# Performance work log

Measured on AMD Instinct MI355X. Metric: run time of the kernel, lower is better.

Reference implementation:

```python
import jax, jax.numpy as jnp
import numpy as np

N_NODES = 100000
N_EDGES = 800000
N_GRAPHS = 16
NFEAT = 128
NHID = 128
NCLASS = 2


def setup_inputs() -> dict:
    key = jax.random.key(0)
    k1, k2, k3, k4, k5, k6, k7 = jax.random.split(key, 7)
    x = jax.random.normal(k1, (N_NODES, NFEAT), dtype=jnp.float32)
    edge_index = jax.random.randint(k2, (2, N_EDGES), 0, N_NODES, dtype=jnp.int64)
    batch = jnp.sort(jax.random.randint(k3, (N_NODES,), 0, N_GRAPHS, dtype=jnp.int64))
    # GCNConv params (glorot-ish scale)
    W1 = jax.random.normal(k4, (NFEAT, NHID), dtype=jnp.float32) / np.sqrt(NFEAT)
    b1 = jnp.zeros((NHID,), dtype=jnp.float32)
    W2 = jax.random.normal(k5, (NHID, NCLASS), dtype=jnp.float32) / np.sqrt(NHID)
    b2 = jnp.zeros((NCLASS,), dtype=jnp.float32)
    return {"x": x, "edge_index": edge_index, "batch": batch,
            "W1": W1, "b1": b1, "W2": W2, "b2": b2}


def _prep_edges(edge_index, n):
    """Add self-loops and compute symmetric GCN normalization."""
    loop = jnp.arange(n, dtype=edge_index.dtype)
    row = jnp.concatenate([edge_index[0], loop])  # source
    col = jnp.concatenate([edge_index[1], loop])  # target
    deg = jax.ops.segment_sum(jnp.ones_like(col, dtype=jnp.float32), col, num_segments=n)
    dinv = jnp.where(deg > 0, jax.lax.rsqrt(deg), 0.0)
    norm = dinv[row] * dinv[col]  # [E+N]
    return row, col, norm


def _gcn_conv(x, row, col, norm, W, b):
    h = x @ W                                  # [N, out]
    msg = h[row] * norm[:, None]               # gather + scale, [E+N, out]
    out = jax.ops.segment_sum(msg, col, num_segments=x.shape[0])  # scatter-add
    return out + b


def reference(x, edge_index, batch, W1, b1, W2, b2):
    n = x.shape[0]
    row, col, norm = _prep_edges(edge_index, n)
    h = jax.nn.relu(_gcn_conv(x, row, col, norm, W1, b1))
    # dropout is identity at inference
    h = _gcn_conv(h, row, col, norm, W2, b2)
    # global_mean_pool over graph ids
    sums = jax.ops.segment_sum(h, batch, num_segments=N_GRAPHS)          # [G, nclass]
    cnts = jax.ops.segment_sum(jnp.ones((n,), h.dtype), batch, num_segments=N_GRAPHS)
    pooled = sums / jnp.maximum(cnts, 1.0)[:, None]
    return jax.nn.log_softmax(pooled, axis=1)
```

## Files before the change

kernel.cpp:

```cpp
#include <hip/hip_runtime.h>
#include <hip/hip_bf16.h>

#define N_NODES 100000
#define N_EDGES 800000
#define N_GRAPHS 16
#define NFEAT 128
#define NHID 128
#define NCLASS 2

#define SCAN_CHUNK 2048
#define NCHUNK ((N_NODES + SCAN_CHUNK - 1) / SCAN_CHUNK)

#define GEMM_BLOCKS 512
#define N_CHUNKS (N_NODES / 16)

#define FILL_BINS 8
#define FILL_SLICES 128
#define FILL_BIN_W (N_NODES / FILL_BINS)
#define FILL_SLICE_E (N_EDGES / FILL_SLICES)

#define P2_BLOCKS 512
#define P2_TPB 1024
#define P2_WAVES (P2_BLOCKS * (P2_TPB / 64))
#define P2_PER ((N_NODES + P2_WAVES - 1) / P2_WAVES)

typedef unsigned int uint32;
typedef __attribute__((ext_vector_type(8))) short short8;
typedef __attribute__((ext_vector_type(4))) float f32x4;
typedef __attribute__((ext_vector_type(2))) float f32x2;

__device__ __forceinline__ unsigned short f2bf(float f) {
  unsigned u = __float_as_uint(f);
  unsigned r = (u + 0x7fffu + ((u >> 16) & 1u)) >> 16;
  return (unsigned short)r;
}
__device__ __forceinline__ uint32 bfpack(float a, float b) {
  return (uint32)f2bf(a) | ((uint32)f2bf(b) << 16);
}
__device__ __forceinline__ float bflo(uint32 u) { return __uint_as_float(u << 16); }
__device__ __forceinline__ float bfhi(uint32 u) { return __uint_as_float(u & 0xffff0000u); }

__global__ void k_deg(const int* __restrict__ ei, int* __restrict__ deg) {
  int e = blockIdx.x * blockDim.x + threadIdx.x;
  if (e < N_EDGES) atomicAdd(&deg[ei[N_EDGES + e]], 1);
}

__global__ void k_scan1(const int* __restrict__ deg, int* __restrict__ csum,
                        float* __restrict__ dinv) {
  __shared__ int lds[256];
  int b = blockIdx.x, t = threadIdx.x;
  int base = b * SCAN_CHUNK + t * 8;
  int s = 0;
#pragma unroll
  for (int k = 0; k < 8; ++k) {
    int i = base + k;
    int d = (i < N_NODES) ? deg[i] : 0;
    if (i < N_NODES) dinv[i] = rsqrtf((float)d + 1.0f);
    s += d;
  }
  lds[t] = s;
  __syncthreads();
  for (int off = 128; off > 0; off >>= 1) {
    if (t < off) lds[t] += lds[t + off];
    __syncthreads();
  }
  if (t == 0) csum[b] = lds[0];
}

__global__ void k_scan3(const int* __restrict__ deg, const int* __restrict__ csum,
                        int* __restrict__ offsets, int* __restrict__ cursor) {
  __shared__ int lds[256];
  __shared__ int soff;
  int b = blockIdx.x, t = threadIdx.x;
  if (t == 0) {
    int run = 0;
    for (int i = 0; i < b; ++i) run += csum[i];
    soff = run;
  }
  int base = b * SCAN_CHUNK + t * 8;
  int v[8];
  int s = 0;
#pragma unroll
  for (int k = 0; k < 8; ++k) {
    int i = base + k;
    v[k] = (i < N_NODES) ? deg[i] : 0;
    s += v[k];
  }
  lds[t] = s;
  __syncthreads();
  int total = s;
  for (int off = 1; off < 256; off <<= 1) {
    int x = (t >= off) ? lds[t - off] : 0;
    __syncthreads();
    lds[t] += x;
    __syncthreads();
  }
  int run = lds[t] - total + soff;
#pragma unroll
  for (int k = 0; k < 8; ++k) {
    int i = base + k;
    if (i < N_NODES) { offsets[i] = run; cursor[i] = run; }
    run += v[k];
  }
}

__global__ __launch_bounds__(256) void k_fill(const int* __restrict__ ei,
                                              int* __restrict__ cursor,
                                              int* __restrict__ csr_row) {
  int bin = blockIdx.x & (FILL_BINS - 1);
  int slice = blockIdx.x >> 3;
  int lo = bin * FILL_BIN_W;
  int hi = lo + FILL_BIN_W;
  int e0 = slice * FILL_SLICE_E;
  int e1 = e0 + FILL_SLICE_E;
  for (int e = e0 + threadIdx.x; e < e1; e += 256) {
    int c = ei[N_EDGES + e];
    if (c >= lo && c < hi) {
      int r = ei[e];
      int p = atomicAdd(&cursor[c], 1);
      csr_row[p] = r;
    }
  }
}

__global__ __launch_bounds__(256, 2) void k_gemm_mfma(const float* __restrict__ x,
                                                      const float* __restrict__ W1,
                                                      const float* __restrict__ dinv,
                                                      unsigned char* __restrict__ xw8) {
  __shared__ __align__(16) unsigned short Wt[128 * 136];
  int t = threadIdx.x;
  for (int i = t; i < 4096; i += 256) {
    float4 w4 = ((const float4*)W1)[i];
    int k = i >> 5;
    int n0 = (i & 31) * 4;
    Wt[(n0 + 0) * 136 + k] = f2bf(w4.x);
    Wt[(n0 + 1) * 136 + k] = f2bf(w4.y);
    Wt[(n0 + 2) * 136 + k] = f2bf(w4.z);
    Wt[(n0 + 3) * 136 + k] = f2bf(w4.w);
  }
  __syncthreads();

  int lane = t & 63;
  int c = lane & 15;
  int quad = lane >> 4;
  short8 b[4][8];
#pragma unroll
  for (int kt = 0; kt < 4; ++kt)
#pragma unroll
    for (int nt = 0; nt < 8; ++nt)
      b[kt][nt] = *(const short8*)&Wt[(nt * 16 + c) * 136 + kt * 32 + quad * 8];

  int wave = blockIdx.x * 4 + (t >> 6);
  for (int chunk = wave; chunk < N_CHUNKS; chunk += GEMM_BLOCKS * 4) {
    const float* xr = x + (size_t)(chunk * 16 + c) * 128 + quad * 8;
    short8 a[4];
#pragma unroll
    for (int kt = 0; kt < 4; ++kt) {
      float4 f0 = *(const float4*)(xr + kt * 32);
      float4 f1 = *(const float4*)(xr + kt * 32 + 4);
      short8 v;
      v[0] = (short)f2bf(f0.x); v[1] = (short)f2bf(f0.y);
      v[2] = (short)f2bf(f0.z); v[3] = (short)f2bf(f0.w);
      v[4] = (short)f2bf(f1.x); v[5] = (short)f2bf(f1.y);
      v[6] = (short)f2bf(f1.z); v[7] = (short)f2bf(f1.w);
      a[kt] = v;
    }
    f32x4 acc[8];
#pragma unroll
    for (int nt = 0; nt < 8; ++nt) acc[nt] = (f32x4)(0.f);
#pragma unroll
    for (int kt = 0; kt < 4; ++kt)
#pragma unroll
      for (int nt = 0; nt < 8; ++nt)
        acc[nt] = __builtin_amdgcn_mfma_f32_16x16x32_bf16(a[kt], b[kt][nt], acc[nt], 0, 0, 0);

    int rbase = chunk * 16 + quad * 4;
    float d0 = dinv[rbase + 0], d1 = dinv[rbase + 1];
    float d2 = dinv[rbase + 2], d3 = dinv[rbase + 3];
#pragma unroll
    for (int nt = 0; nt < 8; ++nt) {
      int cb = nt * 16 + c;
      float v0 = acc[nt][0] * d0, v1 = acc[nt][1] * d1;
      float v2 = acc[nt][2] * d2, v3 = acc[nt][3] * d3;
      int p01 = __builtin_amdgcn_cvt_pk_fp8_f32(v0, v1, 0, false);
      int p23 = __builtin_amdgcn_cvt_pk_fp8_f32(v2, v3, 0, false);
      xw8[(size_t)(rbase + 0) * 128 + cb] = (unsigned char)(p01 & 0xff);
      xw8[(size_t)(rbase + 1) * 128 + cb] = (unsigned char)((p01 >> 8) & 0xff);
      xw8[(size_t)(rbase + 2) * 128 + cb] = (unsigned char)(p23 & 0xff);
      xw8[(size_t)(rbase + 3) * 128 + cb] = (unsigned char)((p23 >> 8) & 0xff);
    }
  }
}

__global__ __launch_bounds__(256) void k_conv1(const unsigned char* __restrict__ xw8,
                                               const int* __restrict__ csr_row,
                                               const int* __restrict__ offsets,
                                               const int* __restrict__ deg,
                                               const float* __restrict__ dinv,
                                               const float* __restrict__ b1,
                                               const float* __restrict__ W2,
                                               float2* __restrict__ h2) {
  int t = threadIdx.x;
  int lane = t & 63;
  int j = lane & 15;
  int gbase = lane & 48;
  int node = blockIdx.x * 16 + (t >> 4);

  int st = offsets[node];
  int cnt = deg[node];

  int ci = min(j, cnt);
  int rj = (ci == 0) ? node : csr_row[st + ci - 1];

  f32x2 acc2[4];
#pragma unroll
  for (int k = 0; k < 4; ++k) acc2[k] = (f32x2)(0.f);

  const uint2* rowp = (const uint2*)xw8;

#pragma unroll
  for (int i = 0; i < 16; ++i) {
    int r = __shfl(rj, gbase + i, 64);
    uint2 u = rowp[(size_t)r * 16 + j];
    if (i > cnt) { u.x = 0u; u.y = 0u; }
    acc2[0] += __builtin_amdgcn_cvt_pk_f32_fp8(u.x, false);
    acc2[1] += __builtin_amdgcn_cvt_pk_f32_fp8(u.x, true);
    acc2[2] += __builtin_amdgcn_cvt_pk_f32_fp8(u.y, false);
    acc2[3] += __builtin_amdgcn_cvt_pk_f32_fp8(u.y, true);
  }

  for (int s = 16; s <= cnt; s += 16) {
    int idx = s + j;
    int ci2 = min(idx, cnt);
    int rj2 = csr_row[st + ci2 - 1];
#pragma unroll
    for (int i = 0; i < 16; ++i) {
      int r = __shfl(rj2, gbase + i, 64);
      uint2 u = rowp[(size_t)r * 16 + j];
      if (s + i > cnt) { u.x = 0u; u.y = 0u; }
      acc2[0] += __builtin_amdgcn_cvt_pk_f32_fp8(u.x, false);
      acc2[1] += __builtin_amdgcn_cvt_pk_f32_fp8(u.x, true);
      acc2[2] += __builtin_amdgcn_cvt_pk_f32_fp8(u.y, false);
      acc2[3] += __builtin_amdgcn_cvt_pk_f32_fp8(u.y, true);
    }
  }

  float dc = dinv[node];
  float4 bA = *(const float4*)(b1 + j * 8);
  float4 bB = *(const float4*)(b1 + j * 8 + 4);
  float o[8];
  o[0] = fmaxf(acc2[0][0] * dc + bA.x, 0.f) * dc;
  o[1] = fmaxf(acc2[0][1] * dc + bA.y, 0.f) * dc;
  o[2] = fmaxf(acc2[1][0] * dc + bA.z, 0.f) * dc;
  o[3] = fmaxf(acc2[1][1] * dc + bA.w, 0.f) * dc;
  o[4] = fmaxf(acc2[2][0] * dc + bB.x, 0.f) * dc;
  o[5] = fmaxf(acc2[2][1] * dc + bB.y, 0.f) * dc;
  o[6] = fmaxf(acc2[3][0] * dc + bB.z, 0.f) * dc;
  o[7] = fmaxf(acc2[3][1] * dc + bB.w, 0.f) * dc;

  const float2* W2v = (const float2*)W2;
  float q0 = 0.f, q1 = 0.f;
#pragma unroll
  for (int k = 0; k < 8; ++k) {
    float2 wv = W2v[j * 8 + k];
    q0 += o[k] * wv.x;
    q1 += o[k] * wv.y;
  }
#pragma unroll
  for (int m = 1; m < 16; m <<= 1) {
    q0 += __shfl_xor(q0, m, 64);
    q1 += __shfl_xor(q1, m, 64);
  }
  if (j == 0) h2[node] = make_float2(q0, q1);
}

__global__ __launch_bounds__(P2_TPB) void k_conv2pool(const float2* __restrict__ h2,
                                                      const int* __restrict__ csr_row,
                                                      const int* __restrict__ offsets,
                                                      const int* __restrict__ deg,
                                                      const float* __restrict__ dinv,
                                                      const int* __restrict__ batch,
                                                      float* __restrict__ partials) {
  __shared__ float sacc[N_GRAPHS * 2];
  int t = threadIdx.x;
  if (t < N_GRAPHS * 2) sacc[t] = 0.f;
  __syncthreads();
  int lane = t & 63;
  int grp = lane >> 4;
  int j = lane & 15;
  int w = blockIdx.x * (P2_TPB / 64) + (t >> 6);
  int n0 = w * P2_PER;
  int n1 = min(n0 + P2_PER, N_NODES);
  float p0 = 0.f, p1 = 0.f;
  int gcur = -1;
  for (int nb = n0; nb < n1; nb += 4) {
    int node = nb + grp;
    bool valid = node < n1;
    int st = 0, cnt = -1;
    if (valid) { st = offsets[node]; cnt = deg[node]; }
    float a0 = 0.f, a1 = 0.f;
    for (int s = 0; s <= cnt; s += 16) {
      int idx = s + j;
      if (idx <= cnt) {
        int r = (idx == 0) ? node : csr_row[st + idx - 1];
        float2 v = h2[r];
        a0 += v.x;
        a1 += v.y;
      }
    }
#pragma unroll
    for (int m = 1; m < 16; m <<= 1) {
      a0 += __shfl_xor(a0, m, 64);
      a1 += __shfl_xor(a1, m, 64);
    }
    if (valid && j == 0) {
      int g = batch[node];
      if (g != gcur) {
        if (gcur >= 0) {
          atomicAdd(&sacc[gcur * 2 + 0], p0);
          atomicAdd(&sacc[gcur * 2 + 1], p1);
        }
        p0 = 0.f; p1 = 0.f;
        gcur = g;
      }
      float dc = dinv[node];
      p0 += a0 * dc;
      p1 += a1 * dc;
    }
  }
  if (gcur >= 0) {
    atomicAdd(&sacc[gcur * 2 + 0], p0);
    atomicAdd(&sacc[gcur * 2 + 1], p1);
  }
  __syncthreads();
  if (t < N_GRAPHS * 2)
    partials[(size_t)blockIdx.x * (N_GRAPHS * 2) + t] = sacc[t];
}

__global__ __launch_bounds__(256) void k_tail(const float* __restrict__ partials,
                                              const int* __restrict__ batch,
                                              const float* __restrict__ b2,
                                              float* __restrict__ out) {
  __shared__ float red[8];
  __shared__ int cntsh;
  int g = blockIdx.x;
  int t = threadIdx.x;
  if (t == 0) {
    int lo = 0, hi = N_NODES;
    while (lo < hi) { int m = (lo + hi) >> 1; if (batch[m] < g) lo = m + 1; else hi = m; }
    int b0 = lo;
    lo = 0; hi = N_NODES;
    while (lo < hi) { int m = (lo + hi) >> 1; if (batch[m] < g + 1) lo = m + 1; else hi = m; }
    cntsh = lo - b0;
  }
  float s0 = 0.f, s1 = 0.f;
  for (int b = t; b < P2_BLOCKS; b += 256) {
    s0 += partials[(size_t)b * (N_GRAPHS * 2) + g * 2 + 0];
    s1 += partials[(size_t)b * (N_GRAPHS * 2) + g * 2 + 1];
  }
#pragma unroll
  for (int m = 1; m < 64; m <<= 1) {
    s0 += __shfl_xor(s0, m, 64);
    s1 += __shfl_xor(s1, m, 64);
  }
  int wv = t >> 6, ln = t & 63;
  if (ln == 0) { red[wv * 2] = s0; red[wv * 2 + 1] = s1; }
  __syncthreads();
  if (t == 0) {
    float p0 = red[0] + red[2] + red[4] + red[6];
    float p1 = red[1] + red[3] + red[5] + red[7];
    float cnt = fmaxf((float)cntsh, 1.0f);
    p0 = p0 / cnt + b2[0];
    p1 = p1 / cnt + b2[1];
    float m = fmaxf(p0, p1);
    float lse = m + logf(expf(p0 - m) + expf(p1 - m));
    out[g * 2 + 0] = p0 - lse;
    out[g * 2 + 1] = p1 - lse;
  }
}

static inline size_t align256(size_t x) { return (x + 255) & ~(size_t)255; }

extern "C" void kernel_launch(void* const* d_in, const int* in_sizes, int n_in,
                              void* d_out, int out_size, void* d_ws, size_t ws_size,
                              hipStream_t stream) {
  (void)in_sizes; (void)n_in; (void)out_size; (void)ws_size;
  const float* x  = (const float*)d_in[0];
  const int*   ei = (const int*)d_in[1];
  const int*   batch = (const int*)d_in[2];
  const float* W1 = (const float*)d_in[3];
  const float* b1 = (const float*)d_in[4];
  const float* W2 = (const float*)d_in[5];
  const float* b2 = (const float*)d_in[6];
  float* out = (float*)d_out;

  char* w = (char*)d_ws;
  size_t off = 0;
  unsigned char* xw8 = (unsigned char*)(w + off); off = align256(off + (size_t)N_NODES * NHID);
  float2* h2 = (float2*)(w + off);       off = align256(off + (size_t)N_NODES * sizeof(float2));
  int* csr_row = (int*)(w + off);        off = align256(off + (size_t)N_EDGES * 4);
  float* partials = (float*)(w + off);   off = align256(off + (size_t)P2_BLOCKS * N_GRAPHS * 2 * 4);
  float* dinv = (float*)(w + off);       off = align256(off + (size_t)N_NODES * 4);
  int* deg = (int*)(w + off);            off = align256(off + (size_t)N_NODES * 4);
  int* cursor = (int*)(w + off);         off = align256(off + (size_t)N_NODES * 4);
  int* offsets = (int*)(w + off);        off = align256(off + (size_t)N_NODES * 4);
  int* csum = (int*)(w + off);           off = align256(off + (size_t)NCHUNK * 4);

  hipMemsetAsync(deg, 0, (size_t)N_NODES * 4, stream);
  k_deg<<<(N_EDGES + 255) / 256, 256, 0, stream>>>(ei, deg);
  k_scan1<<<NCHUNK, 256, 0, stream>>>(deg, csum, dinv);
  k_scan3<<<NCHUNK, 256, 0, stream>>>(deg, csum, offsets, cursor);
  k_fill<<<FILL_BINS * FILL_SLICES, 256, 0, stream>>>(ei, cursor, csr_row);
  k_gemm_mfma<<<GEMM_BLOCKS, 256, 0, stream>>>(x, W1, dinv, xw8);
  k_conv1<<<(N_NODES + 15) / 16, 256, 0, stream>>>(xw8, csr_row, offsets, deg, dinv, b1, W2, h2);
  k_conv2pool<<<P2_BLOCKS, P2_TPB, 0, stream>>>(h2, csr_row, offsets, deg, dinv, batch, partials);
  k_tail<<<N_GRAPHS, 256, 0, stream>>>(partials, batch, b2, out);
}
```

Baseline: 234.1 us.

## Process two nodes per lane group in conv1 and pool layer-2 directly over edges

conv1 now gives each 16-lane group two nodes, interleaving the first 16 neighbour gathers of both nodes so more loads are in flight per wave, with W2 hoisted into registers. The CSR-based second-layer aggregation plus pooling is replaced by an edge-parallel kernel that reads the raw edge list, scales h2[row] by dinv[col] and atomically adds it into per-graph LDS accumulators, with a separate pass for self-loops. This removes the per-node degree imbalance in the second layer, at the cost of heavy LDS atomic contention on only 32 addresses and random reads of batch and dinv per edge.

```diff
diff --git a/kernel.cpp b/kernel.cpp
--- a/kernel.cpp
+++ b/kernel.cpp
@@ -19,10 +19,8 @@
 #define FILL_BIN_W (N_NODES / FILL_BINS)
 #define FILL_SLICE_E (N_EDGES / FILL_SLICES)
 
-#define P2_BLOCKS 512
-#define P2_TPB 1024
-#define P2_WAVES (P2_BLOCKS * (P2_TPB / 64))
-#define P2_PER ((N_NODES + P2_WAVES - 1) / P2_WAVES)
+#define P2E_BLOCKS 1024
+#define P2E_TPB 256
 
 typedef unsigned int uint32;
 typedef __attribute__((ext_vector_type(8))) short short8;
@@ -34,11 +32,6 @@
   unsigned r = (u + 0x7fffu + ((u >> 16) & 1u)) >> 16;
   return (unsigned short)r;
 }
-__device__ __forceinline__ uint32 bfpack(float a, float b) {
-  return (uint32)f2bf(a) | ((uint32)f2bf(b) << 16);
-}
-__device__ __forceinline__ float bflo(uint32 u) { return __uint_as_float(u << 16); }
-__device__ __forceinline__ float bfhi(uint32 u) { return __uint_as_float(u & 0xffff0000u); }
 
 __global__ void k_deg(const int* __restrict__ ei, int* __restrict__ deg) {
   int e = blockIdx.x * blockDim.x + threadIdx.x;
@@ -204,133 +197,142 @@
   int lane = t & 63;
   int j = lane & 15;
   int gbase = lane & 48;
-  int node = blockIdx.x * 16 + (t >> 4);
-
-  int st = offsets[node];
-  int cnt = deg[node];
-
-  int ci = min(j, cnt);
-  int rj = (ci == 0) ? node : csr_row[st + ci - 1];
-
-  f32x2 acc2[4];
-#pragma unroll
-  for (int k = 0; k < 4; ++k) acc2[k] = (f32x2)(0.f);
+  int nA = blockIdx.x * 32 + (t >> 4) * 2;
+  int nB = nA + 1;
+
+  int stA = offsets[nA], cntA = deg[nA];
+  int stB = offsets[nB], cntB = deg[nB];
+
+  int ciA = min(j, cntA);
+  int rjA = (ciA == 0) ? nA : csr_row[stA + ciA - 1];
+  int ciB = min(j, cntB);
+  int rjB = (ciB == 0) ? nB : csr_row[stB + ciB - 1];
+
+  f32x2 aA[4], aB[4];
+#pragma unroll
+  for (int k = 0; k < 4; ++k) { aA[k] = (f32x2)(0.f); aB[k] = (f32x2)(0.f); }
 
   const uint2* rowp = (const uint2*)xw8;
 
 #pragma unroll
   for (int i = 0; i < 16; ++i) {
-    int r = __shfl(rj, gbase + i, 64);
-    uint2 u = rowp[(size_t)r * 16 + j];
-    if (i > cnt) { u.x = 0u; u.y = 0u; }
-    acc2[0] += __builtin_amdgcn_cvt_pk_f32_fp8(u.x, false);
-    acc2[1] += __builtin_amdgcn_cvt_pk_f32_fp8(u.x, true);
-    acc2[2] += __builtin_amdgcn_cvt_pk_f32_fp8(u.y, false);
-    acc2[3] += __builtin_amdgcn_cvt_pk_f32_fp8(u.y, true);
-  }
-
-  for (int s = 16; s <= cnt; s += 16) {
-    int idx = s + j;
-    int ci2 = min(idx, cnt);
-    int rj2 = csr_row[st + ci2 - 1];
+    int rA = __shfl(rjA, gbase + i, 64);
+    int rB = __shfl(rjB, gbase + i, 64);
+    uint2 uA = rowp[(size_t)rA * 16 + j];
+    uint2 uB = rowp[(size_t)rB * 16 + j];
+    if (i > cntA) { uA.x = 0u; uA.y = 0u; }
+    if (i > cntB) { uB.x = 0u; uB.y = 0u; }
+    aA[0] += __builtin_amdgcn_cvt_pk_f32_fp8(uA.x, false);
+    aA[1] += __builtin_amdgcn_cvt_pk_f32_fp8(uA.x, true);
+    aA[2] += __builtin_amdgcn_cvt_pk_f32_fp8(uA.y, false);
+    aA[3] += __builtin_amdgcn_cvt_pk_f32_fp8(uA.y, true);
+    aB[0] += __builtin_amdgcn_cvt_pk_f32_fp8(uB.x, false);
+    aB[1] += __builtin_amdgcn_cvt_pk_f32_fp8(uB.x, true);
+    aB[2] += __builtin_amdgcn_cvt_pk_f32_fp8(uB.y, false);
+    aB[3] += __builtin_amdgcn_cvt_pk_f32_fp8(uB.y, true);
+  }
+
+  for (int s = 16; s <= cntA; s += 16) {
+    int ci2 = min(s + j, cntA);
+    int rj2 = csr_row[stA + ci2 - 1];
 #pragma unroll
     for (int i = 0; i < 16; ++i) {
       int r = __shfl(rj2, gbase + i, 64);
       uint2 u = rowp[(size_t)r * 16 + j];
-      if (s + i > cnt) { u.x = 0u; u.y = 0u; }
-      acc2[0] += __builtin_amdgcn_cvt_pk_f32_fp8(u.x, false);
-      acc2[1] += __builtin_amdgcn_cvt_pk_f32_fp8(u.x, true);
-      acc2[2] += __builtin_amdgcn_cvt_pk_f32_fp8(u.y, false);
-      acc2[3] += __builtin_amdgcn_cvt_pk_f32_fp8(u.y, true);
+      if (s + i > cntA) { u.x = 0u; u.y = 0u; }
+      aA[0] += __builtin_amdgcn_cvt_pk_f32_fp8(u.x, false);
+      aA[1] += __builtin_amdgcn_cvt_pk_f32_fp8(u.x, true);
+      aA[2] += __builtin_amdgcn_cvt_pk_f32_fp8(u.y, false);
+      aA[3] += __builtin_amdgcn_cvt_pk_f32_fp8(u.y, true);
     }
   }
-
-  float dc = dinv[node];
-  float4 bA = *(const float4*)(b1 + j * 8);
-  float4 bB = *(const float4*)(b1 + j * 8 + 4);
-  float o[8];
-  o[0] = fmaxf(acc2[0][0] * dc + bA.x, 0.f) * dc;
-  o[1] = fmaxf(acc2[0][1] * dc + bA.y, 0.f) * dc;
-  o[2] = fmaxf(acc2[1][0] * dc + bA.z, 0.f) * dc;
-  o[3] = fmaxf(acc2[1][1] * dc + bA.w, 0.f) * dc;
-  o[4] = fmaxf(acc2[2][0] * dc + bB.x, 0.f) * dc;
-  o[5] = fmaxf(acc2[2][1] * dc + bB.y, 0.f) * dc;
-  o[6] = fmaxf(acc2[3][0] * dc + bB.z, 0.f) * dc;
-  o[7] = fmaxf(acc2[3][1] * dc + bB.w, 0.f) * dc;
-
+  for (int s = 16; s <= cntB; s += 16) {
+    int ci2 = min(s + j, cntB);
+    int rj2 = csr_row[stB + ci2 - 1];
+#pragma unroll
+    for (int i = 0; i < 16; ++i) {
+      int r = __shfl(rj2, gbase + i, 64);
+      uint2 u = rowp[(size_t)r * 16 + j];
+      if (s + i > cntB) { u.x = 0u; u.y = 0u; }
+      aB[0] += __builtin_amdgcn_cvt_pk_f32_fp8(u.x, false);
+      aB[1] += __builtin_amdgcn_cvt_pk_f32_fp8(u.x, true);
+      aB[2] += __builtin_amdgcn_cvt_pk_f32_fp8(u.y, false);
+      aB[3] += __builtin_amdgcn_cvt_pk_f32_fp8(u.y, true);
+    }
+  }
+
+  float4 bA4 = *(const float4*)(b1 + j * 8);
+  float4 bB4 = *(const float4*)(b1 + j * 8 + 4);
   const float2* W2v = (const float2*)W2;
-  float q0 = 0.f, q1 = 0.f;
-#pragma unroll
-  for (int k = 0; k < 8; ++k) {
-    float2 wv = W2v[j * 8 + k];
-    q0 += o[k] * wv.x;
-    q1 += o[k] * wv.y;
+  float2 w2r[8];
+#pragma unroll
+  for (int k = 0; k < 8; ++k) w2r[k] = W2v[j * 8 + k];
+
+  float dA = dinv[nA], dB = dinv[nB];
+  float qA0 = 0.f, qA1 = 0.f, qB0 = 0.f, qB1 = 0.f;
+  {
+    float o[8];
+    o[0] = fmaxf(aA[0][0] * dA + bA4.x, 0.f) * dA;
+    o[1] = fmaxf(aA[0][1] * dA + bA4.y, 0.f) * dA;
+    o[2] = fmaxf(aA[1][0] * dA + bA4.z, 0.f) * dA;
+    o[3] = fmaxf(aA[1][1] * dA + bA4.w, 0.f) * dA;
+    o[4] = fmaxf(aA[2][0] * dA + bB4.x, 0.f) * dA;
+    o[5] = fmaxf(aA[2][1] * dA + bB4.y, 0.f) * dA;
+    o[6] = fmaxf(aA[3][0] * dA + bB4.z, 0.f) * dA;
+    o[7] = fmaxf(aA[3][1] * dA + bB4.w, 0.f) * dA;
+#pragma unroll
+    for (int k = 0; k < 8; ++k) { qA0 += o[k] * w2r[k].x; qA1 += o[k] * w2r[k].y; }
+  }
+  {
+    float o[8];
+    o[0] = fmaxf(aB[0][0] * dB + bA4.x, 0.f) * dB;
+    o[1] = fmaxf(aB[0][1] * dB + bA4.y, 0.f) * dB;
+    o[2] = fmaxf(aB[1][0] * dB + bA4.z, 0.f) * dB;
+    o[3] = fmaxf(aB[1][1] * dB + bA4.w, 0.f) * dB;
+    o[4] = fmaxf(aB[2][0] * dB + bB4.x, 0.f) * dB;
+    o[5] = fmaxf(aB[2][1] * dB + bB4.y, 0.f) * dB;
+    o[6] = fmaxf(aB[3][0] * dB + bB4.z, 0.f) * dB;
+    o[7] = fmaxf(aB[3][1] * dB + bB4.w, 0.f) * dB;
+#pragma unroll
+    for (int k = 0; k < 8; ++k) { qB0 += o[k] * w2r[k].x; qB1 += o[k] * w2r[k].y; }
   }
 #pragma unroll
   for (int m = 1; m < 16; m <<= 1) {
-    q0 += __shfl_xor(q0, m, 64);
-    q1 += __shfl_xor(q1, m, 64);
-  }
-  if (j == 0) h2[node] = make_float2(q0, q1);
-}
-
-__global__ __launch_bounds__(P2_TPB) void k_conv2pool(const float2* __restrict__ h2,
-                                                      const int* __restrict__ csr_row,
-                                                      const int* __restrict__ offsets,
-                                                      const int* __restrict__ deg,
-                                                      const float* __restrict__ dinv,
-                                                      const int* __restrict__ batch,
-                                                      float* __restrict__ partials) {
+    qA0 += __shfl_xor(qA0, m, 64);
+    qA1 += __shfl_xor(qA1, m, 64);
+    qB0 += __shfl_xor(qB0, m, 64);
+    qB1 += __shfl_xor(qB1, m, 64);
+  }
+  if (j == 0) h2[nA] = make_float2(qA0, qA1);
+  if (j == 1) h2[nB] = make_float2(qB0, qB1);
+}
+
+__global__ __launch_bounds__(P2E_TPB) void k_pool_edges(const float2* __restrict__ h2,
+                                                        const int* __restrict__ ei,
+                                                        const int* __restrict__ batch,
+                                                        const float* __restrict__ dinv,
+                                                        float* __restrict__ partials) {
   __shared__ float sacc[N_GRAPHS * 2];
   int t = threadIdx.x;
   if (t < N_GRAPHS * 2) sacc[t] = 0.f;
   __syncthreads();
-  int lane = t & 63;
-  int grp = lane >> 4;
-  int j = lane & 15;
-  int w = blockIdx.x * (P2_TPB / 64) + (t >> 6);
-  int n0 = w * P2_PER;
-  int n1 = min(n0 + P2_PER, N_NODES);
-  float p0 = 0.f, p1 = 0.f;
-  int gcur = -1;
-  for (int nb = n0; nb < n1; nb += 4) {
-    int node = nb + grp;
-    bool valid = node < n1;
-    int st = 0, cnt = -1;
-    if (valid) { st = offsets[node]; cnt = deg[node]; }
-    float a0 = 0.f, a1 = 0.f;
-    for (int s = 0; s <= cnt; s += 16) {
-      int idx = s + j;
-      if (idx <= cnt) {
-        int r = (idx == 0) ? node : csr_row[st + idx - 1];
-        float2 v = h2[r];
-        a0 += v.x;
-        a1 += v.y;
-      }
-    }
-#pragma unroll
-    for (int m = 1; m < 16; m <<= 1) {
-      a0 += __shfl_xor(a0, m, 64);
-      a1 += __shfl_xor(a1, m, 64);
-    }
-    if (valid && j == 0) {
-      int g = batch[node];
-      if (g != gcur) {
-        if (gcur >= 0) {
-          atomicAdd(&sacc[gcur * 2 + 0], p0);
-          atomicAdd(&sacc[gcur * 2 + 1], p1);
-        }
-        p0 = 0.f; p1 = 0.f;
-        gcur = g;
-      }
-      float dc = dinv[node];
-      p0 += a0 * dc;
-      p1 += a1 * dc;
-    }
-  }
-  if (gcur >= 0) {
-    atomicAdd(&sacc[gcur * 2 + 0], p0);
-    atomicAdd(&sacc[gcur * 2 + 1], p1);
+  int tid = blockIdx.x * P2E_TPB + t;
+  int stride = P2E_BLOCKS * P2E_TPB;
+  for (int e = tid; e < N_EDGES; e += stride) {
+    int r = ei[e];
+    int c = ei[N_EDGES + e];
+    float2 v = h2[r];
+    float dc = dinv[c];
+    int g = batch[c];
+    atomicAdd(&sacc[g * 2 + 0], v.x * dc);
+    atomicAdd(&sacc[g * 2 + 1], v.y * dc);
+  }
+  for (int n = tid; n < N_NODES; n += stride) {
+    float2 v = h2[n];
+    float dn = dinv[n];
+    int g = batch[n];
+    atomicAdd(&sacc[g * 2 + 0], v.x * dn);
+    atomicAdd(&sacc[g * 2 + 1], v.y * dn);
   }
   __syncthreads();
   if (t < N_GRAPHS * 2)
@@ -354,7 +356,7 @@
     cntsh = lo - b0;
   }
   float s0 = 0.f, s1 = 0.f;
-  for (int b = t; b < P2_BLOCKS; b += 256) {
+  for (int b = t; b < P2E_BLOCKS; b += 256) {
     s0 += partials[(size_t)b * (N_GRAPHS * 2) + g * 2 + 0];
     s1 += partials[(size_t)b * (N_GRAPHS * 2) + g * 2 + 1];
   }
@@ -399,7 +401,7 @@
   unsigned char* xw8 = (unsigned char*)(w + off); off = align256(off + (size_t)N_NODES * NHID);
   float2* h2 = (float2*)(w + off);       off = align256(off + (size_t)N_NODES * sizeof(float2));
   int* csr_row = (int*)(w + off);        off = align256(off + (size_t)N_EDGES * 4);
-  float* partials = (float*)(w + off);   off = align256(off + (size_t)P2_BLOCKS * N_GRAPHS * 2 * 4);
+  float* partials = (float*)(w + off);   off = align256(off + (size_t)P2E_BLOCKS * N_GRAPHS * 2 * 4);
   float* dinv = (float*)(w + off);       off = align256(off + (size_t)N_NODES * 4);
   int* deg = (int*)(w + off);            off = align256(off + (size_t)N_NODES * 4);
   int* cursor = (int*)(w + off);         off = align256(off + (size_t)N_NODES * 4);
@@ -412,7 +414,7 @@
   k_scan3<<<NCHUNK, 256, 0, stream>>>(deg, csum, offsets, cursor);
   k_fill<<<FILL_BINS * FILL_SLICES, 256, 0, stream>>>(ei, cursor, csr_row);
   k_gemm_mfma<<<GEMM_BLOCKS, 256, 0, stream>>>(x, W1, dinv, xw8);
-  k_conv1<<<(N_NODES + 15) / 16, 256, 0, stream>>>(xw8, csr_row, offsets, deg, dinv, b1, W2, h2);
-  k_conv2pool<<<P2_BLOCKS, P2_TPB, 0, stream>>>(h2, csr_row, offsets, deg, dinv, batch, partials);
+  k_conv1<<<N_NODES / 32, 256, 0, stream>>>(xw8, csr_row, offsets, deg, dinv, b1, W2, h2);
+  k_pool_edges<<<P2E_BLOCKS, P2E_TPB, 0, stream>>>(h2, ei, batch, dinv, partials);
   k_tail<<<N_GRAPHS, 256, 0, stream>>>(partials, batch, b2, out);
 }
```

Measured after the change: 238.7 us. No clear change (+1.9%).

## Pack fp8 GEMM output stores and pool second layer by edge-parallel scatter

Applied to the files above, without the earlier changes.

The GEMM epilogue now packs eight fp8 values per row into one 8-byte store instead of scattered byte stores. This permutes the feature layout inside each row, so conv1 now indexes b1 and W2 with a strided feature mapping to match. The CSR-based conv2-plus-pool kernel is replaced by an edge-parallel kernel that reads the raw edge list and accumulates into 16 graph bins with shared-memory atomics. This removes per-node gather imbalance but adds heavy atomic contention on 32 LDS addresses and random reads of h2, dinv and batch.

```diff
diff --git a/kernel.cpp b/kernel.cpp
--- a/kernel.cpp
+++ b/kernel.cpp
@@ -19,10 +19,8 @@
 #define FILL_BIN_W (N_NODES / FILL_BINS)
 #define FILL_SLICE_E (N_EDGES / FILL_SLICES)
 
-#define P2_BLOCKS 512
-#define P2_TPB 1024
-#define P2_WAVES (P2_BLOCKS * (P2_TPB / 64))
-#define P2_PER ((N_NODES + P2_WAVES - 1) / P2_WAVES)
+#define P2E_BLOCKS 1024
+#define P2E_TPB 256
 
 typedef unsigned int uint32;
 typedef __attribute__((ext_vector_type(8))) short short8;
@@ -30,15 +28,11 @@
 typedef __attribute__((ext_vector_type(2))) float f32x2;
 
 __device__ __forceinline__ unsigned short f2bf(float f) {
-  unsigned u = __float_as_uint(f);
-  unsigned r = (u + 0x7fffu + ((u >> 16) & 1u)) >> 16;
-  return (unsigned short)r;
-}
-__device__ __forceinline__ uint32 bfpack(float a, float b) {
-  return (uint32)f2bf(a) | ((uint32)f2bf(b) << 16);
-}
-__device__ __forceinline__ float bflo(uint32 u) { return __uint_as_float(u << 16); }
-__device__ __forceinline__ float bfhi(uint32 u) { return __uint_as_float(u & 0xffff0000u); }
+  __hip_bfloat16 h = __float2bfloat16(f);
+  unsigned short r;
+  __builtin_memcpy(&r, &h, 2);
+  return r;
+}
 
 __global__ void k_deg(const int* __restrict__ ei, int* __restrict__ deg) {
   int e = blockIdx.x * blockDim.x + threadIdx.x;
@@ -175,19 +169,17 @@
         acc[nt] = __builtin_amdgcn_mfma_f32_16x16x32_bf16(a[kt], b[kt][nt], acc[nt], 0, 0, 0);
 
     int rbase = chunk * 16 + quad * 4;
-    float d0 = dinv[rbase + 0], d1 = dinv[rbase + 1];
-    float d2 = dinv[rbase + 2], d3 = dinv[rbase + 3];
-#pragma unroll
-    for (int nt = 0; nt < 8; ++nt) {
-      int cb = nt * 16 + c;
-      float v0 = acc[nt][0] * d0, v1 = acc[nt][1] * d1;
-      float v2 = acc[nt][2] * d2, v3 = acc[nt][3] * d3;
-      int p01 = __builtin_amdgcn_cvt_pk_fp8_f32(v0, v1, 0, false);
-      int p23 = __builtin_amdgcn_cvt_pk_fp8_f32(v2, v3, 0, false);
-      xw8[(size_t)(rbase + 0) * 128 + cb] = (unsigned char)(p01 & 0xff);
-      xw8[(size_t)(rbase + 1) * 128 + cb] = (unsigned char)((p01 >> 8) & 0xff);
-      xw8[(size_t)(rbase + 2) * 128 + cb] = (unsigned char)(p23 & 0xff);
-      xw8[(size_t)(rbase + 3) * 128 + cb] = (unsigned char)((p23 >> 8) & 0xff);
+#pragma unroll
+    for (int r = 0; r < 4; ++r) {
+      float d = dinv[rbase + r];
+      int w0 = __builtin_amdgcn_cvt_pk_fp8_f32(acc[0][r] * d, acc[1][r] * d, 0, false);
+      w0 = __builtin_amdgcn_cvt_pk_fp8_f32(acc[2][r] * d, acc[3][r] * d, w0, true);
+      int w1 = __builtin_amdgcn_cvt_pk_fp8_f32(acc[4][r] * d, acc[5][r] * d, 0, false);
+      w1 = __builtin_amdgcn_cvt_pk_fp8_f32(acc[6][r] * d, acc[7][r] * d, w1, true);
+      uint2 st;
+      st.x = (uint32)w0;
+      st.y = (uint32)w1;
+      *(uint2*)&xw8[(size_t)(rbase + r) * 128 + c * 8] = st;
     }
   }
 }
@@ -246,25 +238,15 @@
   }
 
   float dc = dinv[node];
-  float4 bA = *(const float4*)(b1 + j * 8);
-  float4 bB = *(const float4*)(b1 + j * 8 + 4);
-  float o[8];
-  o[0] = fmaxf(acc2[0][0] * dc + bA.x, 0.f) * dc;
-  o[1] = fmaxf(acc2[0][1] * dc + bA.y, 0.f) * dc;
-  o[2] = fmaxf(acc2[1][0] * dc + bA.z, 0.f) * dc;
-  o[3] = fmaxf(acc2[1][1] * dc + bA.w, 0.f) * dc;
-  o[4] = fmaxf(acc2[2][0] * dc + bB.x, 0.f) * dc;
-  o[5] = fmaxf(acc2[2][1] * dc + bB.y, 0.f) * dc;
-  o[6] = fmaxf(acc2[3][0] * dc + bB.z, 0.f) * dc;
-  o[7] = fmaxf(acc2[3][1] * dc + bB.w, 0.f) * dc;
-
+  float q0 = 0.f, q1 = 0.f;
   const float2* W2v = (const float2*)W2;
-  float q0 = 0.f, q1 = 0.f;
 #pragma unroll
   for (int k = 0; k < 8; ++k) {
-    float2 wv = W2v[j * 8 + k];
-    q0 += o[k] * wv.x;
-    q1 += o[k] * wv.y;
+    float a = acc2[k >> 1][k & 1];
+    float ok = fmaxf(a * dc + b1[k * 16 + j], 0.f) * dc;
+    float2 wv = W2v[k * 16 + j];
+    q0 += ok * wv.x;
+    q1 += ok * wv.y;
   }
 #pragma unroll
   for (int m = 1; m < 16; m <<= 1) {
@@ -274,63 +256,32 @@
   if (j == 0) h2[node] = make_float2(q0, q1);
 }
 
-__global__ __launch_bounds__(P2_TPB) void k_conv2pool(const float2* __restrict__ h2,
-                                                      const int* __restrict__ csr_row,
-                                                      const int* __restrict__ offsets,
-                                                      const int* __restrict__ deg,
-                                                      const float* __restrict__ dinv,
-                                                      const int* __restrict__ batch,
-                                                      float* __restrict__ partials) {
+__global__ __launch_bounds__(P2E_TPB) void k_pool_edges(const float2* __restrict__ h2,
+                                                        const int* __restrict__ ei,
+                                                        const int* __restrict__ batch,
+                                                        const float* __restrict__ dinv,
+                                                        float* __restrict__ partials) {
   __shared__ float sacc[N_GRAPHS * 2];
   int t = threadIdx.x;
   if (t < N_GRAPHS * 2) sacc[t] = 0.f;
   __syncthreads();
-  int lane = t & 63;
-  int grp = lane >> 4;
-  int j = lane & 15;
-  int w = blockIdx.x * (P2_TPB / 64) + (t >> 6);
-  int n0 = w * P2_PER;
-  int n1 = min(n0 + P2_PER, N_NODES);
-  float p0 = 0.f, p1 = 0.f;
-  int gcur = -1;
-  for (int nb = n0; nb < n1; nb += 4) {
-    int node = nb + grp;
-    bool valid = node < n1;
-    int st = 0, cnt = -1;
-    if (valid) { st = offsets[node]; cnt = deg[node]; }
-    float a0 = 0.f, a1 = 0.f;
-    for (int s = 0; s <= cnt; s += 16) {
-      int idx = s + j;
-      if (idx <= cnt) {
-        int r = (idx == 0) ? node : csr_row[st + idx - 1];
-        float2 v = h2[r];
-        a0 += v.x;
-        a1 += v.y;
-      }
-    }
-#pragma unroll
-    for (int m = 1; m < 16; m <<= 1) {
-      a0 += __shfl_xor(a0, m, 64);
-      a1 += __shfl_xor(a1, m, 64);
-    }
-    if (valid && j == 0) {
-      int g = batch[node];
-      if (g != gcur) {
-        if (gcur >= 0) {
-          atomicAdd(&sacc[gcur * 2 + 0], p0);
-          atomicAdd(&sacc[gcur * 2 + 1], p1);
-        }
-        p0 = 0.f; p1 = 0.f;
-        gcur = g;
-      }
-      float dc = dinv[node];
-      p0 += a0 * dc;
-      p1 += a1 * dc;
-    }
-  }
-  if (gcur >= 0) {
-    atomicAdd(&sacc[gcur * 2 + 0], p0);
-    atomicAdd(&sacc[gcur * 2 + 1], p1);
+  int tid = blockIdx.x * P2E_TPB + t;
+  int stride = P2E_BLOCKS * P2E_TPB;
+  for (int e = tid; e < N_EDGES; e += stride) {
+    int r = ei[e];
+    int c = ei[N_EDGES + e];
+    float2 v = h2[r];
+    float dc = dinv[c];
+    int g = batch[c];
+    atomicAdd(&sacc[g * 2 + 0], v.x * dc);
+    atomicAdd(&sacc[g * 2 + 1], v.y * dc);
+  }
+  for (int n = tid; n < N_NODES; n += stride) {
+    float2 v = h2[n];
+    float dn = dinv[n];
+    int g = batch[n];
+    atomicAdd(&sacc[g * 2 + 0], v.x * dn);
+    atomicAdd(&sacc[g * 2 + 1], v.y * dn);
   }
   __syncthreads();
   if (t < N_GRAPHS * 2)
@@ -354,7 +305,7 @@
     cntsh = lo - b0;
   }
   float s0 = 0.f, s1 = 0.f;
-  for (int b = t; b < P2_BLOCKS; b += 256) {
+  for (int b = t; b < P2E_BLOCKS; b += 256) {
     s0 += partials[(size_t)b * (N_GRAPHS * 2) + g * 2 + 0];
     s1 += partials[(size_t)b * (N_GRAPHS * 2) + g * 2 + 1];
   }
@@ -399,7 +350,7 @@
   unsigned char* xw8 = (unsigned char*)(w + off); off = align256(off + (size_t)N_NODES * NHID);
   float2* h2 = (float2*)(w + off);       off = align256(off + (size_t)N_NODES * sizeof(float2));
   int* csr_row = (int*)(w + off);        off = align256(off + (size_t)N_EDGES * 4);
-  float* partials = (float*)(w + off);   off = align256(off + (size_t)P2_BLOCKS * N_GRAPHS * 2 * 4);
+  float* partials = (float*)(w + off);   off = align256(off + (size_t)P2E_BLOCKS * N_GRAPHS * 2 * 4);
   float* dinv = (float*)(w + off);       off = align256(off + (size_t)N_NODES * 4);
   int* deg = (int*)(w + off);            off = align256(off + (size_t)N_NODES * 4);
   int* cursor = (int*)(w + off);         off = align256(off + (size_t)N_NODES * 4);
@@ -412,7 +363,7 @@
   k_scan3<<<NCHUNK, 256, 0, stream>>>(deg, csum, offsets, cursor);
   k_fill<<<FILL_BINS * FILL_SLICES, 256, 0, stream>>>(ei, cursor, csr_row);
   k_gemm_mfma<<<GEMM_BLOCKS, 256, 0, stream>>>(x, W1, dinv, xw8);
-  k_conv1<<<(N_NODES + 15) / 16, 256, 0, stream>>>(xw8, csr_row, offsets, deg, dinv, b1, W2, h2);
-  k_conv2pool<<<P2_BLOCKS, P2_TPB, 0, stream>>>(h2, csr_row, offsets, deg, dinv, batch, partials);
+  k_conv1<<<N_NODES / 16, 256, 0, stream>>>(xw8, csr_row, offsets, deg, dinv, b1, W2, h2);
+  k_pool_edges<<<P2E_BLOCKS, P2E_TPB, 0, stream>>>(h2, ei, batch, dinv, partials);
   k_tail<<<N_GRAPHS, 256, 0, stream>>>(partials, batch, b2, out);
 }
```

Result: no change. 236.3 us (+0.9%).
